# Kernel optimization log

Hardware: AMD Instinct MI355X
Metric: run time of the kernel (lower is better)

## Reference

```python
import jax, jax.numpy as jnp
import numpy as np

TOP_K = 2

def setup_inputs() -> dict:
    key = jax.random.key(0)
    k1, k2, k3, k4 = jax.random.split(key, 4)
    B, T, C = 4, 2048, 1024
    E, D_FF = 8, 1024  # d_ff = 1 * n_embd
    x = jax.random.normal(k1, (B, T, C), dtype=jnp.float32)
    router_w = jax.random.normal(k2, (E, C), dtype=jnp.float32) * 0.02
    w1 = jax.random.normal(k3, (E, C, D_FF), dtype=jnp.float32) * 0.02
    w2 = jax.random.normal(k4, (E, D_FF, C), dtype=jnp.float32) * 0.02
    return {"x": x, "router_w": router_w, "w1": w1, "w2": w2}

def reference(x, router_w, w1, w2):
    B, T, C = x.shape
    x_flat = x.reshape(-1, C)                          # [N, C]
    logits = x_flat @ router_w.T                       # [N, E]
    probs = jax.nn.softmax(logits, axis=-1)
    weights, indices = jax.lax.top_k(probs, TOP_K)     # [N, K], [N, K]
    # Dense per-expert compute (same math as gathering w1/w2 per token,
    # without duplicating weight slices per token).
    hidden = jax.nn.relu(jnp.einsum('nc,ecf->nef', x_flat, w1))  # [N, E, d_ff]
    out_all = jnp.einsum('nef,efc->nec', hidden, w2)             # [N, E, C]
    sel = jnp.take_along_axis(out_all, indices[:, :, None], axis=1)  # [N, K, C]
    out = jnp.sum(sel * weights[:, :, None], axis=1)   # [N, C]
    return out.reshape(B, T, C)
```

## Files before the change

### kernel.cpp

```cpp
#include <hip/hip_runtime.h>
#include <hip/hip_bf16.h>

#define NTOK 8192
#define CDIM 1024
#define FDIM 1024
#define NEXP 8
#define BM 128
#define BN 128
#define BK 64
#define NKT (CDIM / BK)
#define MAXT 136
#define NWG (8 * MAXT)

typedef __attribute__((ext_vector_type(8))) short short8;
typedef __attribute__((ext_vector_type(4))) float f32x4;

union Pack4 { __hip_bfloat16 h[4]; unsigned long long v; };
union U4 { unsigned long long u; unsigned short s[4]; };

typedef const unsigned int __attribute__((address_space(1)))* gas_ptr;
typedef unsigned int __attribute__((address_space(3)))* las_ptr;

__device__ __forceinline__ void gload16(const void* g, void* l) {
    __builtin_amdgcn_global_load_lds(
        (gas_ptr)(unsigned long long)g,
        (las_ptr)(unsigned int)(unsigned long long)l,
        16, 0, 0);
}

__device__ __forceinline__ float bf2f(unsigned short v) {
    unsigned int t = (unsigned int)v << 16;
    return __uint_as_float(t);
}

__global__ __launch_bounds__(256) void router_kernel(
    const float* __restrict__ x, const float* __restrict__ rw,
    __hip_bfloat16* __restrict__ xb,
    int* __restrict__ cnt, int* __restrict__ rows, float* __restrict__ wts)
{
    __shared__ int lcnt[NEXP];
    __shared__ int lt[NEXP][32];
    __shared__ float lw[NEXP][32];
    __shared__ int base[NEXP];
    const int tid = threadIdx.x;
    const int wv = tid >> 6, lane = tid & 63;
    if (tid < NEXP) lcnt[tid] = 0;
    __syncthreads();

    for (int tt = 0; tt < 4; tt++) {
        const int n = blockIdx.x * 16 + wv * 4 + tt;
        float acc[NEXP];
#pragma unroll
        for (int e = 0; e < NEXP; e++) acc[e] = 0.f;
#pragma unroll
        for (int c0 = 0; c0 < CDIM; c0 += 256) {
            const size_t o = (size_t)n * CDIM + c0 + lane * 4;
            float4 xv = *(const float4*)(x + o);
            Pack4 p4;
            p4.h[0] = __float2bfloat16(xv.x); p4.h[1] = __float2bfloat16(xv.y);
            p4.h[2] = __float2bfloat16(xv.z); p4.h[3] = __float2bfloat16(xv.w);
            *(unsigned long long*)(xb + o) = p4.v;
#pragma unroll
            for (int e = 0; e < NEXP; e++) {
                float4 w4 = *(const float4*)&rw[e * CDIM + c0 + lane * 4];
                acc[e] += xv.x * w4.x + xv.y * w4.y + xv.z * w4.z + xv.w * w4.w;
            }
        }
#pragma unroll
        for (int e = 0; e < NEXP; e++) {
#pragma unroll
            for (int s = 32; s > 0; s >>= 1) acc[e] += __shfl_xor(acc[e], s);
        }
        if (lane == 0) {
            float mx = acc[0];
#pragma unroll
            for (int e = 1; e < NEXP; e++) mx = fmaxf(mx, acc[e]);
            float p[NEXP], se = 0.f;
#pragma unroll
            for (int e = 0; e < NEXP; e++) { p[e] = __expf(acc[e] - mx); se += p[e]; }
            float inv = 1.f / se;
            int i0 = 0;
#pragma unroll
            for (int e = 1; e < NEXP; e++) if (p[e] > p[i0]) i0 = e;
            int i1 = (i0 == 0) ? 1 : 0;
#pragma unroll
            for (int e = 0; e < NEXP; e++) if (e != i0 && p[e] > p[i1]) i1 = e;
            int p0 = atomicAdd(&lcnt[i0], 1);
            lt[i0][p0] = n;
            lw[i0][p0] = p[i0] * inv;
            int p1 = atomicAdd(&lcnt[i1], 1);
            lt[i1][p1] = n | (1 << 16);
            lw[i1][p1] = p[i1] * inv;
        }
    }
    __syncthreads();
    if (tid < NEXP) base[tid] = atomicAdd(&cnt[tid * 16], lcnt[tid]);
    __syncthreads();
#pragma unroll
    for (int e = 0; e < NEXP; e++) {
        for (int i = tid; i < lcnt[e]; i += 256) {
            rows[e * NTOK + base[e] + i] = lt[e][i];
            wts [e * NTOK + base[e] + i] = lw[e][i];
        }
    }
}

__global__ void scan_offsets(const int* __restrict__ cnt, int* __restrict__ offs,
                             int* __restrict__ wl)
{
    if (threadIdx.x == 0) {
        int s = 0, t = 0;
        for (int e = 0; e < NEXP; e++) {
            int me = cnt[e * 16];
            offs[e] = s; s += me;
            for (int m0 = 0; m0 < me; m0 += BM) {
                wl[1 + 2 * t] = e; wl[2 + 2 * t] = m0; t++;
            }
        }
        wl[0] = t;
    }
}

__global__ __launch_bounds__(256) void build_slots(
    const int* __restrict__ cnt, const int* __restrict__ offs,
    const int* __restrict__ rows, int* __restrict__ slot)
{
    const int e = blockIdx.y;
    const int i = blockIdx.x * 256 + threadIdx.x;
    if (i < cnt[e * 16]) {
        int p = rows[e * NTOK + i];
        slot[2 * (p & 0xFFFF) + (p >> 16)] = offs[e] + i;
    }
}

__global__ __launch_bounds__(256) void transpose_conv(
    const float* __restrict__ src, __hip_bfloat16* __restrict__ dst)
{
    __shared__ float t[32][33];
    const int e = blockIdx.z;
    const int r0 = blockIdx.x * 32, c0 = blockIdx.y * 32;
    const int tid = threadIdx.x;
    const int rr = tid >> 3;
    const int cc = (tid & 7) * 4;
    const float* p = src + ((size_t)e * 1024 + r0 + rr) * 1024 + c0 + cc;
    float4 v = *(const float4*)p;
    t[rr][cc] = v.x; t[rr][cc + 1] = v.y; t[rr][cc + 2] = v.z; t[rr][cc + 3] = v.w;
    __syncthreads();
    const int cr = tid >> 3;
    const int rc = (tid & 7) * 4;
    Pack4 o;
#pragma unroll
    for (int j = 0; j < 4; j++) o.h[j] = __float2bfloat16(t[rc + j][cr]);
    *(unsigned long long*)(dst + ((size_t)e * 1024 + c0 + cr) * 1024 + r0 + rc) = o.v;
}

__global__ __launch_bounds__(256, 2) void moe_gemm1(
    const __hip_bfloat16* __restrict__ xb, const __hip_bfloat16* __restrict__ w1t,
    const int* __restrict__ cnt, const int* __restrict__ offs,
    const int* __restrict__ wl, const int* __restrict__ rows,
    __hip_bfloat16* __restrict__ hid)
{
    const int bid = blockIdx.x;
    const int wid = (bid & 7) * MAXT + (bid >> 3);
    const int t = wid >> 3;
    if (t >= wl[0]) return;
    const int n0 = (wid & 7) * BN;
    const int e = wl[1 + 2 * t], m0 = wl[2 + 2 * t];
    const int me = cnt[e * 16], off = offs[e];
    const int tid = threadIdx.x;
    const int lane = tid & 63, wv = tid >> 6;
    const int wr = wv >> 1, wc = wv & 1;
    const int fr = lane & 15, fq = lane >> 4;
    const int fx = fr & 7;

    __shared__ alignas(16) __hip_bfloat16 smem[2][2][BM * BK];

    const int swz8 = (((lane & 7) ^ (lane >> 3))) * 8;
    const __hip_bfloat16* asrc[4];
    const __hip_bfloat16* bsrc[4];
#pragma unroll
    for (int i = 0; i < 4; i++) {
        int row = i * 32 + wv * 8 + (lane >> 3);
        int gi = m0 + row;
        int ri = gi < me ? gi : me - 1;
        int tok = rows[e * NTOK + ri] & 0xFFFF;
        asrc[i] = xb + (size_t)tok * CDIM + swz8;
        bsrc[i] = w1t + ((size_t)e * FDIM + n0 + row) * CDIM + swz8;
    }

    f32x4 acc[4][4] = {};

#pragma unroll
    for (int i = 0; i < 4; i++) {
        gload16(asrc[i], &smem[0][0][(i * 256 + wv * 64) * 8]);
        gload16(bsrc[i], &smem[0][1][(i * 256 + wv * 64) * 8]);
    }
    __syncthreads();

    int cur = 0;
    for (int kt = 0; kt < NKT; kt++) {
        if (kt + 1 < NKT) {
            const int k1 = (kt + 1) * BK;
#pragma unroll
            for (int i = 0; i < 4; i++) {
                gload16(asrc[i] + k1, &smem[cur ^ 1][0][(i * 256 + wv * 64) * 8]);
                gload16(bsrc[i] + k1, &smem[cur ^ 1][1][(i * 256 + wv * 64) * 8]);
            }
        }
#pragma unroll
        for (int ks = 0; ks < 2; ks++) {
            short8 af[4], bfv[4];
#pragma unroll
            for (int m = 0; m < 4; m++)
                af[m] = *(const short8*)&smem[cur][0][
                    (wr * 64 + m * 16 + fr) * BK + (((ks * 4 + fq) ^ fx) * 8)];
#pragma unroll
            for (int n = 0; n < 4; n++)
                bfv[n] = *(const short8*)&smem[cur][1][
                    (wc * 64 + n * 16 + fr) * BK + (((ks * 4 + fq) ^ fx) * 8)];
#pragma unroll
            for (int m = 0; m < 4; m++)
#pragma unroll
                for (int n = 0; n < 4; n++)
                    acc[m][n] = __builtin_amdgcn_mfma_f32_16x16x32_bf16(
                        af[m], bfv[n], acc[m][n], 0, 0, 0);
        }
        __syncthreads();
        cur ^= 1;
    }

    __hip_bfloat16 (*Cl)[BN] = reinterpret_cast<__hip_bfloat16(*)[BN]>(&smem[0][0][0]);
#pragma unroll
    for (int m = 0; m < 4; m++)
#pragma unroll
        for (int n = 0; n < 4; n++)
#pragma unroll
            for (int r = 0; r < 4; r++) {
                int il = wr * 64 + m * 16 + fq * 4 + r;
                float v = acc[m][n][r];
                Cl[il][wc * 64 + n * 16 + fr] = __float2bfloat16(v > 0.f ? v : 0.f);
            }
    __syncthreads();
#pragma unroll
    for (int i = 0; i < 8; i++) {
        int chunk = i * 256 + tid;
        int row = chunk >> 4, c8 = (chunk & 15) * 8;
        int gi = m0 + row;
        if (gi < me)
            *(short8*)(hid + (size_t)(off + gi) * FDIM + n0 + c8) =
                *(const short8*)&Cl[row][c8];
    }
}

__global__ __launch_bounds__(256, 2) void moe_gemm2(
    const __hip_bfloat16* __restrict__ hid, const __hip_bfloat16* __restrict__ w2t,
    const int* __restrict__ cnt, const int* __restrict__ offs,
    const int* __restrict__ wl, const int* __restrict__ rows,
    const float* __restrict__ wts, __hip_bfloat16* __restrict__ ybuf,
    float* __restrict__ out)
{
    const int bid = blockIdx.x;
    const int wid = (bid & 7) * MAXT + (bid >> 3);
    const int t = wid >> 3;
    if (t >= wl[0]) return;
    const int n0 = (wid & 7) * BN;
    const int e = wl[1 + 2 * t], m0 = wl[2 + 2 * t];
    const int me = cnt[e * 16], off = offs[e];
    const int tid = threadIdx.x;
    const int lane = tid & 63, wv = tid >> 6;
    const int wr = wv >> 1, wc = wv & 1;
    const int fr = lane & 15, fq = lane >> 4;
    const int fx = fr & 7;

    __shared__ alignas(16) __hip_bfloat16 smem[2][2][BM * BK];
    __shared__ int rtok[BM];
    __shared__ float rwt[BM];

    if (tid < BM) {
        int gi = m0 + tid;
        int ri = gi < me ? gi : me - 1;
        rtok[tid] = rows[e * NTOK + ri] & 0xFFFF;
        rwt[tid] = gi < me ? wts[e * NTOK + ri] : 0.f;
    }

    const int swz8 = (((lane & 7) ^ (lane >> 3))) * 8;
    const __hip_bfloat16* asrc[4];
    const __hip_bfloat16* bsrc[4];
#pragma unroll
    for (int i = 0; i < 4; i++) {
        int row = i * 32 + wv * 8 + (lane >> 3);
        int gi = m0 + row;
        int ri = gi < me ? gi : me - 1;
        asrc[i] = hid + (size_t)(off + ri) * FDIM + swz8;
        bsrc[i] = w2t + ((size_t)e * CDIM + n0 + row) * FDIM + swz8;
    }

    f32x4 acc[4][4] = {};

#pragma unroll
    for (int i = 0; i < 4; i++) {
        gload16(asrc[i], &smem[0][0][(i * 256 + wv * 64) * 8]);
        gload16(bsrc[i], &smem[0][1][(i * 256 + wv * 64) * 8]);
    }
    __syncthreads();

    int cur = 0;
    for (int kt = 0; kt < NKT; kt++) {
        if (kt + 1 < NKT) {
            const int k1 = (kt + 1) * BK;
#pragma unroll
            for (int i = 0; i < 4; i++) {
                gload16(asrc[i] + k1, &smem[cur ^ 1][0][(i * 256 + wv * 64) * 8]);
                gload16(bsrc[i] + k1, &smem[cur ^ 1][1][(i * 256 + wv * 64) * 8]);
            }
        }
#pragma unroll
        for (int ks = 0; ks < 2; ks++) {
            short8 af[4], bfv[4];
#pragma unroll
            for (int m = 0; m < 4; m++)
                af[m] = *(const short8*)&smem[cur][0][
                    (wr * 64 + m * 16 + fr) * BK + (((ks * 4 + fq) ^ fx) * 8)];
#pragma unroll
            for (int n = 0; n < 4; n++)
                bfv[n] = *(const short8*)&smem[cur][1][
                    (wc * 64 + n * 16 + fr) * BK + (((ks * 4 + fq) ^ fx) * 8)];
#pragma unroll
            for (int m = 0; m < 4; m++)
#pragma unroll
                for (int n = 0; n < 4; n++)
                    acc[m][n] = __builtin_amdgcn_mfma_f32_16x16x32_bf16(
                        af[m], bfv[n], acc[m][n], 0, 0, 0);
        }
        __syncthreads();
        cur ^= 1;
    }

    if (ybuf) {
        __hip_bfloat16 (*Cl)[BN] = reinterpret_cast<__hip_bfloat16(*)[BN]>(&smem[0][0][0]);
#pragma unroll
        for (int m = 0; m < 4; m++)
#pragma unroll
            for (int n = 0; n < 4; n++)
#pragma unroll
                for (int r = 0; r < 4; r++) {
                    int il = wr * 64 + m * 16 + fq * 4 + r;
                    Cl[il][wc * 64 + n * 16 + fr] =
                        __float2bfloat16(rwt[il] * acc[m][n][r]);
                }
        __syncthreads();
#pragma unroll
        for (int i = 0; i < 8; i++) {
            int chunk = i * 256 + tid;
            int row = chunk >> 4, c8 = (chunk & 15) * 8;
            int gi = m0 + row;
            if (gi < me)
                *(short8*)(ybuf + (size_t)(off + gi) * CDIM + n0 + c8) =
                    *(const short8*)&Cl[row][c8];
        }
    } else {
#pragma unroll
        for (int m = 0; m < 4; m++)
#pragma unroll
            for (int n = 0; n < 4; n++)
#pragma unroll
                for (int r = 0; r < 4; r++) {
                    int il = wr * 64 + m * 16 + fq * 4 + r;
                    int gi = m0 + il;
                    if (gi < me)
                        atomicAdd(&out[(size_t)rtok[il] * CDIM + n0 + wc * 64 + n * 16 + fr],
                                  rwt[il] * acc[m][n][r]);
                }
    }
}

__global__ __launch_bounds__(256) void gather_out(
    const __hip_bfloat16* __restrict__ yb, const int* __restrict__ slot,
    float* __restrict__ out)
{
    for (int n = blockIdx.x; n < NTOK; n += gridDim.x) {
        const int s0 = slot[2 * n], s1 = slot[2 * n + 1];
        const int c = threadIdx.x * 4;
        U4 a, b;
        a.u = *(const unsigned long long*)(yb + (size_t)s0 * CDIM + c);
        b.u = *(const unsigned long long*)(yb + (size_t)s1 * CDIM + c);
        float4 o;
        o.x = bf2f(a.s[0]) + bf2f(b.s[0]);
        o.y = bf2f(a.s[1]) + bf2f(b.s[1]);
        o.z = bf2f(a.s[2]) + bf2f(b.s[2]);
        o.w = bf2f(a.s[3]) + bf2f(b.s[3]);
        *(float4*)(out + (size_t)n * CDIM + c) = o;
    }
}

extern "C" void kernel_launch(void* const* d_in, const int* in_sizes, int n_in,
                              void* d_out, int out_size, void* d_ws, size_t ws_size,
                              hipStream_t stream)
{
    const float* x  = (const float*)d_in[0];
    const float* rw = (const float*)d_in[1];
    const float* w1 = (const float*)d_in[2];
    const float* w2 = (const float*)d_in[3];
    float* out = (float*)d_out;
    char* ws = (char*)d_ws;

    int* cnt  = (int*)ws;
    int* offs = (int*)(ws + 1024);
    int* wl   = (int*)(ws + 2048);
    int* rows = (int*)(ws + 4096);
    float* wts = (float*)(ws + 4096 + NEXP * NTOK * 4);
    int* slot = (int*)(ws + 4096 + 2 * NEXP * NTOK * 4);
    __hip_bfloat16* xb  = (__hip_bfloat16*)(ws + (1u << 20));
    __hip_bfloat16* w1t = (__hip_bfloat16*)(ws + (17u << 20));
    __hip_bfloat16* hid = (__hip_bfloat16*)(ws + (33u << 20));
    __hip_bfloat16* w2t = w1t;
    const bool big = ws_size >= ((size_t)98 << 20);
    __hip_bfloat16* ybuf = big ? (__hip_bfloat16*)(ws + (65u << 20)) : nullptr;

    hipMemsetAsync(cnt, 0, 1024, stream);
    if (!big)
        hipMemsetAsync(d_out, 0, (size_t)out_size * sizeof(float), stream);

    router_kernel<<<NTOK / 16, 256, 0, stream>>>(x, rw, xb, cnt, rows, wts);
    scan_offsets<<<1, 64, 0, stream>>>(cnt, offs, wl);
    build_slots<<<dim3(NTOK / 256, NEXP), 256, 0, stream>>>(cnt, offs, rows, slot);
    transpose_conv<<<dim3(32, 32, NEXP), 256, 0, stream>>>(w1, w1t);
    moe_gemm1<<<NWG, 256, 0, stream>>>(xb, w1t, cnt, offs, wl, rows, hid);
    transpose_conv<<<dim3(32, 32, NEXP), 256, 0, stream>>>(w2, w2t);
    moe_gemm2<<<NWG, 256, 0, stream>>>(hid, w2t, cnt, offs, wl, rows, wts, ybuf, out);
    if (big)
        gather_out<<<2048, 256, 0, stream>>>(ybuf, slot, out);
}
```

Before: 165.3 us.

## Replace per-iteration syncthreads with explicit vmcnt waits and enlarge transpose tiles

In both expert GEMM kernels the end-of-iteration __syncthreads is replaced by a barrier at loop top, an explicit s_waitcnt vmcnt(8) that waits only for the previous stage's async LDS loads, and a second barrier. The goal is to let the next tile's global-to-LDS loads stay in flight while the current tile is computed, instead of draining all memory ops at each sync. The weight transpose/convert kernel now uses 64x64 tiles with four loads per thread, which cuts block count and amortises the tile sync. The hand-written waitcnt values assume a specific count of outstanding loads, so a compiler change in instruction emission could break correctness.

Measured after the change: 160.8 us. 1.03x faster.

```diff
diff --git a/kernel.cpp b/kernel.cpp
--- a/kernel.cpp
+++ b/kernel.cpp
@@ -136,22 +136,27 @@
 __global__ __launch_bounds__(256) void transpose_conv(
     const float* __restrict__ src, __hip_bfloat16* __restrict__ dst)
 {
-    __shared__ float t[32][33];
+    __shared__ float t[64][65];
     const int e = blockIdx.z;
-    const int r0 = blockIdx.x * 32, c0 = blockIdx.y * 32;
+    const int r0 = blockIdx.x * 64, c0 = blockIdx.y * 64;
     const int tid = threadIdx.x;
-    const int rr = tid >> 3;
-    const int cc = (tid & 7) * 4;
-    const float* p = src + ((size_t)e * 1024 + r0 + rr) * 1024 + c0 + cc;
-    float4 v = *(const float4*)p;
-    t[rr][cc] = v.x; t[rr][cc + 1] = v.y; t[rr][cc + 2] = v.z; t[rr][cc + 3] = v.w;
-    __syncthreads();
-    const int cr = tid >> 3;
-    const int rc = (tid & 7) * 4;
-    Pack4 o;
-#pragma unroll
-    for (int j = 0; j < 4; j++) o.h[j] = __float2bfloat16(t[rc + j][cr]);
-    *(unsigned long long*)(dst + ((size_t)e * 1024 + c0 + cr) * 1024 + r0 + rc) = o.v;
+    const int rr = tid >> 4;
+    const int cc = (tid & 15) * 4;
+#pragma unroll
+    for (int j = 0; j < 4; j++) {
+        int row = j * 16 + rr;
+        float4 v = *(const float4*)(src + ((size_t)e * 1024 + r0 + row) * 1024 + c0 + cc);
+        t[row][cc] = v.x; t[row][cc + 1] = v.y; t[row][cc + 2] = v.z; t[row][cc + 3] = v.w;
+    }
+    __syncthreads();
+#pragma unroll
+    for (int j = 0; j < 4; j++) {
+        int trow = j * 16 + rr;
+        Pack4 o;
+#pragma unroll
+        for (int k = 0; k < 4; k++) o.h[k] = __float2bfloat16(t[cc + k][trow]);
+        *(unsigned long long*)(dst + ((size_t)e * 1024 + c0 + trow) * 1024 + r0 + cc) = o.v;
+    }
 }
 
 __global__ __launch_bounds__(256, 2) void moe_gemm1(
@@ -195,10 +200,11 @@
         gload16(asrc[i], &smem[0][0][(i * 256 + wv * 64) * 8]);
         gload16(bsrc[i], &smem[0][1][(i * 256 + wv * 64) * 8]);
     }
-    __syncthreads();
+    asm volatile("s_waitcnt lgkmcnt(0)" ::: "memory");
 
     int cur = 0;
     for (int kt = 0; kt < NKT; kt++) {
+        __builtin_amdgcn_s_barrier();
         if (kt + 1 < NKT) {
             const int k1 = (kt + 1) * BK;
 #pragma unroll
@@ -206,7 +212,12 @@
                 gload16(asrc[i] + k1, &smem[cur ^ 1][0][(i * 256 + wv * 64) * 8]);
                 gload16(bsrc[i] + k1, &smem[cur ^ 1][1][(i * 256 + wv * 64) * 8]);
             }
-        }
+            asm volatile("s_waitcnt vmcnt(8)" ::: "memory");
+        } else {
+            asm volatile("s_waitcnt vmcnt(0)" ::: "memory");
+        }
+        __builtin_amdgcn_s_barrier();
+        __builtin_amdgcn_sched_barrier(0);
 #pragma unroll
         for (int ks = 0; ks < 2; ks++) {
             short8 af[4], bfv[4];
@@ -225,9 +236,9 @@
                     acc[m][n] = __builtin_amdgcn_mfma_f32_16x16x32_bf16(
                         af[m], bfv[n], acc[m][n], 0, 0, 0);
         }
-        __syncthreads();
         cur ^= 1;
     }
+    __syncthreads();
 
     __hip_bfloat16 (*Cl)[BN] = reinterpret_cast<__hip_bfloat16(*)[BN]>(&smem[0][0][0]);
 #pragma unroll
@@ -302,10 +313,11 @@
         gload16(asrc[i], &smem[0][0][(i * 256 + wv * 64) * 8]);
         gload16(bsrc[i], &smem[0][1][(i * 256 + wv * 64) * 8]);
     }
-    __syncthreads();
+    asm volatile("s_waitcnt lgkmcnt(0)" ::: "memory");
 
     int cur = 0;
     for (int kt = 0; kt < NKT; kt++) {
+        __builtin_amdgcn_s_barrier();
         if (kt + 1 < NKT) {
             const int k1 = (kt + 1) * BK;
 #pragma unroll
@@ -313,7 +325,12 @@
                 gload16(asrc[i] + k1, &smem[cur ^ 1][0][(i * 256 + wv * 64) * 8]);
                 gload16(bsrc[i] + k1, &smem[cur ^ 1][1][(i * 256 + wv * 64) * 8]);
             }
-        }
+            asm volatile("s_waitcnt vmcnt(8)" ::: "memory");
+        } else {
+            asm volatile("s_waitcnt vmcnt(0)" ::: "memory");
+        }
+        __builtin_amdgcn_s_barrier();
+        __builtin_amdgcn_sched_barrier(0);
 #pragma unroll
         for (int ks = 0; ks < 2; ks++) {
             short8 af[4], bfv[4];
@@ -332,9 +349,9 @@
                     acc[m][n] = __builtin_amdgcn_mfma_f32_16x16x32_bf16(
                         af[m], bfv[n], acc[m][n], 0, 0, 0);
         }
-        __syncthreads();
         cur ^= 1;
     }
+    __syncthreads();
 
     if (ybuf) {
         __hip_bfloat16 (*Cl)[BN] = reinterpret_cast<__hip_bfloat16(*)[BN]>(&smem[0][0][0]);
@@ -424,9 +441,9 @@
     router_kernel<<<NTOK / 16, 256, 0, stream>>>(x, rw, xb, cnt, rows, wts);
     scan_offsets<<<1, 64, 0, stream>>>(cnt, offs, wl);
     build_slots<<<dim3(NTOK / 256, NEXP), 256, 0, stream>>>(cnt, offs, rows, slot);
-    transpose_conv<<<dim3(32, 32, NEXP), 256, 0, stream>>>(w1, w1t);
+    transpose_conv<<<dim3(16, 16, NEXP), 256, 0, stream>>>(w1, w1t);
     moe_gemm1<<<NWG, 256, 0, stream>>>(xb, w1t, cnt, offs, wl, rows, hid);
-    transpose_conv<<<dim3(32, 32, NEXP), 256, 0, stream>>>(w2, w2t);
+    transpose_conv<<<dim3(16, 16, NEXP), 256, 0, stream>>>(w2, w2t);
     moe_gemm2<<<NWG, 256, 0, stream>>>(hid, w2t, cnt, offs, wl, rows, wts, ybuf, out);
     if (big)
         gather_out<<<2048, 256, 0, stream>>>(ybuf, slot, out);
```
